# Kernel optimization log

Hardware: AMD Instinct MI355X
Metric: run time of the kernel (lower is better)

Reference implementation:

```python
import jax, jax.numpy as jnp
import numpy as np

N, E, G, D, L, T = 50000, 100000, 2000, 300, 5, 10
NUM_ATOM, NUM_CHIR, NUM_BOND, NUM_DIR = 120, 3, 6, 3


def setup_inputs() -> dict:
    key = jax.random.key(0)
    ks = jax.random.split(key, 24)
    s = 1.0 / np.sqrt(D)
    inp = {
        'x': jnp.stack([jax.random.randint(ks[0], (N,), 0, NUM_ATOM),
                        jax.random.randint(ks[1], (N,), 0, NUM_CHIR)], axis=1),
        'edge_index': jax.random.randint(ks[2], (2, E), 0, N),
        'edge_attr': jnp.stack([jax.random.randint(ks[3], (E,), 0, 4),
                                jax.random.randint(ks[4], (E,), 0, NUM_DIR)], axis=1),
        'batch': jnp.sort(jax.random.randint(ks[5], (N,), 0, G)),
        'x1': jnp.stack([jax.random.randint(ks[6], (N,), 0, NUM_ATOM),
                         jax.random.randint(ks[7], (N,), 0, NUM_CHIR)], axis=1),
        'edge_index1': jax.random.randint(ks[8], (2, E), 0, N),
        'edge_attr1': jnp.stack([jax.random.randint(ks[9], (E,), 0, 4),
                                 jax.random.randint(ks[10], (E,), 0, NUM_DIR)], axis=1),
        'batch1': jnp.sort(jax.random.randint(ks[11], (N,), 0, G)),
        'xemb1': jax.random.normal(ks[12], (NUM_ATOM, D)) * s,
        'xemb2': jax.random.normal(ks[13], (NUM_CHIR, D)) * s,
        'eemb1': jax.random.normal(ks[14], (L, NUM_BOND, D)) * s,
        'eemb2': jax.random.normal(ks[15], (L, NUM_DIR, D)) * s,
        'W1': jax.random.normal(ks[16], (L, D, 2 * D)) * s,
        'b1': jnp.zeros((L, 2 * D)),
        'W2': jax.random.normal(ks[17], (L, 2 * D, D)) * (1.0 / np.sqrt(2 * D)),
        'b2': jnp.zeros((L, D)),
        'gamma': jnp.ones((L, D)),
        'beta': jnp.zeros((L, D)),
        'predW': jax.random.normal(ks[18], (D, T)) * s,
        'predb': jnp.zeros((T,)),
    }
    return inp


def _gnn(xi, ei, ea, xemb1, xemb2, eemb1, eemb2, W1, b1, W2, b2, gamma, beta):
    n = xi.shape[0]
    h = xemb1[xi[:, 0]] + xemb2[xi[:, 1]]  # [N, D]
    loop = jnp.arange(n)
    src = jnp.concatenate([ei[0], loop])
    dst = jnp.concatenate([ei[1], loop])
    # self-loop edge attr = [4, 0]
    sl = jnp.concatenate([jnp.full((n, 1), 4, ea.dtype), jnp.zeros((n, 1), ea.dtype)], axis=1)
    eaf = jnp.concatenate([ea, sl], axis=0)
    for l in range(L):
        eemb = eemb1[l][eaf[:, 0]] + eemb2[l][eaf[:, 1]]     # [E+N, D]
        msg = h[src] + eemb                                   # gather
        agg = jax.ops.segment_sum(msg, dst, num_segments=n)   # scatter-add
        h2 = jax.nn.relu(agg @ W1[l] + b1[l]) @ W2[l] + b2[l] # GIN MLP
        mu = h2.mean(axis=0)
        var = ((h2 - mu) ** 2).mean(axis=0)                   # batchnorm (train stats)
        h2 = gamma[l] * (h2 - mu) * jax.lax.rsqrt(var + 1e-5) + beta[l]
        if l < L - 1:
            h2 = jax.nn.relu(h2)
        h = h2
    return h  # JK='last'


def _mean_pool(node_rep, batch):
    s = jax.ops.segment_sum(node_rep, batch, num_segments=G)
    cnt = jax.ops.segment_sum(jnp.ones((node_rep.shape[0],), node_rep.dtype), batch, num_segments=G)
    return s / jnp.maximum(cnt, 1.0)[:, None]


def reference(x, edge_index, edge_attr, batch, x1, edge_index1, edge_attr1, batch1,
              xemb1, xemb2, eemb1, eemb2, W1, b1, W2, b2, gamma, beta, predW, predb):
    node_rep = _gnn(x, edge_index, edge_attr, xemb1, xemb2, eemb1, eemb2, W1, b1, W2, b2, gamma, beta)
    node_rep1 = _gnn(x1, edge_index1, edge_attr1, xemb1, xemb2, eemb1, eemb2, W1, b1, W2, b2, gamma, beta)
    graph_rep = _mean_pool(node_rep, batch)
    graph_rep1 = _mean_pool(node_rep1, batch1)
    pred = graph_rep @ predW + predb
    pred1 = graph_rep1 @ predW + predb
    return (pred, graph_rep, node_rep, pred1, graph_rep1, node_rep1)
```

## Files before the change

kernel.cpp:

```cpp
#include <hip/hip_runtime.h>
#include <hip/hip_bf16.h>

typedef unsigned short ushort_t;
typedef short v8s __attribute__((ext_vector_type(8)));
typedef unsigned short v8u __attribute__((ext_vector_type(8)));
typedef unsigned short v4u __attribute__((ext_vector_type(4)));
typedef float v4f __attribute__((ext_vector_type(4)));

#define N_NODES 50000
#define N_EDGES 100000
#define N_GRAPH 2000
#define DIM     300
#define DIM2    600
#define NLAYER  5
#define NTASK   10
#define D4      75
#define D4P     80

#define LDA  304
#define NPAD 50048
#define KST1 10
#define KST2 19

#define KB1 40
#define NT1 5
#define KB2 76
#define NT2 3
#define MT_TILES 391
#define MT2      782

#define AS1 __attribute__((address_space(1)))
#define AS3 __attribute__((address_space(3)))
static __device__ __forceinline__ void gload_lds16(const void* g, void* l) {
    __builtin_amdgcn_global_load_lds((AS1 void*)(g), (AS3 void*)(l), 16, 0, 0);
}

static __device__ __forceinline__ ushort_t f2bf(float f) {
    unsigned int u;
    __builtin_memcpy(&u, &f, 4);
    unsigned int lsb = (u >> 16) & 1u;
    u += 0x7fffu + lsb;
    return (ushort_t)(u >> 16);
}
static __device__ __forceinline__ void split2(float f, ushort_t& h, ushort_t& l) {
    unsigned int u;
    __builtin_memcpy(&u, &f, 4);
    h = (ushort_t)(u >> 16);
    unsigned int um = u & 0xFFFF0000u;
    float hf;
    __builtin_memcpy(&hf, &um, 4);
    float lf = f - hf;
    unsigned int ul;
    __builtin_memcpy(&ul, &lf, 4);
    l = (ushort_t)(ul >> 16);
}

static __device__ __forceinline__ int swz_wgid(int orig, int nwg) {
    int xcd = orig & 7;
    int seq = orig >> 3;
    int q = nwg >> 3, r = nwg & 7;
    int base = (xcd < r) ? xcd * (q + 1) : r * (q + 1) + (xcd - r) * q;
    return base + seq;
}

__global__ void k_deg(const int* __restrict__ ei, int* __restrict__ deg) {
    int e = blockIdx.x * blockDim.x + threadIdx.x;
    if (e >= N_EDGES) return;
    atomicAdd(&deg[ei[N_EDGES + e]], 1);
}

__global__ void k_scan1(const int* __restrict__ deg, int* __restrict__ excl,
                        int* __restrict__ blksum) {
    __shared__ int s[256];
    int i = blockIdx.x * 256 + threadIdx.x;
    int v = (i < N_NODES) ? deg[i] : 0;
    s[threadIdx.x] = v;
    __syncthreads();
#pragma unroll
    for (int o = 1; o < 256; o <<= 1) {
        int t = (threadIdx.x >= o) ? s[threadIdx.x - o] : 0;
        __syncthreads();
        s[threadIdx.x] += t;
        __syncthreads();
    }
    if (i < N_NODES) excl[i] = s[threadIdx.x] - v;
    if (threadIdx.x == 255) blksum[blockIdx.x] = s[255];
}

__global__ void k_scan2(int* __restrict__ blksum, int* __restrict__ blkoff, int nblk) {
    __shared__ int s[256];
    int v = (threadIdx.x < nblk) ? blksum[threadIdx.x] : 0;
    s[threadIdx.x] = v;
    __syncthreads();
#pragma unroll
    for (int o = 1; o < 256; o <<= 1) {
        int t = (threadIdx.x >= o) ? s[threadIdx.x - o] : 0;
        __syncthreads();
        s[threadIdx.x] += t;
        __syncthreads();
    }
    if (threadIdx.x < nblk) blkoff[threadIdx.x] = s[threadIdx.x] - v;
}

__global__ void k_scan3(const int* __restrict__ excl, const int* __restrict__ blkoff,
                        int* __restrict__ rowptr, int* __restrict__ fillptr) {
    int i = blockIdx.x * blockDim.x + threadIdx.x;
    if (i > N_NODES) return;
    int v = (i < N_NODES) ? (excl[i] + blkoff[i >> 8]) : N_EDGES;
    rowptr[i] = v;
    if (i < N_NODES) fillptr[i] = v;
}

__global__ void k_fill(const int* __restrict__ ei, const int* __restrict__ ea,
                       int* __restrict__ fillptr,
                       int* __restrict__ csrc, int* __restrict__ cea) {
    int e = blockIdx.x * blockDim.x + threadIdx.x;
    if (e >= N_EDGES) return;
    int dst = ei[N_EDGES + e];
    int pos = atomicAdd(&fillptr[dst], 1);
    csrc[pos] = ei[e];
    cea[pos] = (ea[2 * e + 0] << 16) | ea[2 * e + 1];
}

template <bool EMB>
__global__ void k_gather_agg(const int* __restrict__ rowptr0,
                             const int* __restrict__ csrc0,
                             const int* __restrict__ cea0,
                             const int* __restrict__ rowptr1,
                             const int* __restrict__ csrc1,
                             const int* __restrict__ cea1,
                             const int* __restrict__ x0,
                             const int* __restrict__ x1,
                             const float* __restrict__ xe1,
                             const float* __restrict__ xe2,
                             const float* __restrict__ hin,
                             const float* __restrict__ ee1,
                             const float* __restrict__ ee2,
                             const float* __restrict__ ee1sl,
                             const float* __restrict__ ee2sl,
                             const float* __restrict__ bnmean,
                             const float* __restrict__ bnrstd,
                             const float* __restrict__ bngam,
                             const float* __restrict__ bnbet,
                             ushort_t* __restrict__ aghi,
                             ushort_t* __restrict__ aglo) {
    int tid = blockIdx.x * blockDim.x + threadIdx.x;
    if (tid >= 2 * N_NODES * D4P) return;
    int gi = tid / D4P;
    int c = tid % D4P;
    int graph = (gi >= N_NODES) ? 1 : 0;
    int ln = gi - graph * N_NODES;
    int row = graph * NPAD + ln;
    int d0 = c * 4;
    const int mt = row >> 7, m = row & 127;
    const int ks = d0 >> 5, kb = (d0 >> 3) & 3, jq = d0 & 7;
    const size_t off = (((size_t)mt * KST1 + ks) * 4 + kb) * 1024 + m * 8 + jq;
    if (c >= D4) {
        v4u z = (v4u){0, 0, 0, 0};
        *(v4u*)(aghi + off) = z;
        *(v4u*)(aglo + off) = z;
        return;
    }
    const int* rowptr = graph ? rowptr1 : rowptr0;
    const int* csrc   = graph ? csrc1   : csrc0;
    const int* cea    = graph ? cea1    : cea0;
    const int* xp     = graph ? x1      : x0;

    float4 m4, r4, g4, b4;
    if (!EMB) {
        const int bo = graph * DIM + d0;
        m4 = *(const float4*)(bnmean + bo);
        r4 = *(const float4*)(bnrstd + bo);
        g4 = *(const float4*)(bngam + d0);
        b4 = *(const float4*)(bnbet + d0);
    }
    auto hval = [&](int node) -> float4 {
        if (EMB) {
            int i0 = xp[node * 2 + 0];
            int i1 = xp[node * 2 + 1];
            float4 a = *(const float4*)(xe1 + (size_t)i0 * DIM + d0);
            float4 b = *(const float4*)(xe2 + (size_t)i1 * DIM + d0);
            float4 o;
            o.x = a.x + b.x; o.y = a.y + b.y; o.z = a.z + b.z; o.w = a.w + b.w;
            return o;
        } else {
            float4 v = *(const float4*)(hin + (size_t)(graph * NPAD + node) * LDA + d0);
            v.x = fmaxf((v.x - m4.x) * r4.x * g4.x + b4.x, 0.f);
            v.y = fmaxf((v.y - m4.y) * r4.y * g4.y + b4.y, 0.f);
            v.z = fmaxf((v.z - m4.z) * r4.z * g4.z + b4.z, 0.f);
            v.w = fmaxf((v.w - m4.w) * r4.w * g4.w + b4.w, 0.f);
            return v;
        }
    };
    float4 a = hval(ln);
    float4 e1 = *(const float4*)(ee1sl + d0);
    float4 e2 = *(const float4*)(ee2sl + d0);
    a.x += e1.x + e2.x; a.y += e1.y + e2.y; a.z += e1.z + e2.z; a.w += e1.w + e2.w;
    int p0 = rowptr[ln], p1 = rowptr[ln + 1];
    for (int p = p0; p < p1; ++p) {
        int src = csrc[p];
        int pk = cea[p];
        int a0 = pk >> 16, a1 = pk & 0xFFFF;
        float4 hv = hval(src);
        float4 f1 = *(const float4*)(ee1 + (size_t)a0 * DIM + d0);
        float4 f2 = *(const float4*)(ee2 + (size_t)a1 * DIM + d0);
        a.x += hv.x + f1.x + f2.x;
        a.y += hv.y + f1.y + f2.y;
        a.z += hv.z + f1.z + f2.z;
        a.w += hv.w + f1.w + f2.w;
    }
    float av[4] = {a.x, a.y, a.z, a.w};
    v4u hh, ll;
#pragma unroll
    for (int i = 0; i < 4; ++i) {
        ushort_t uh, ul;
        split2(av[i], uh, ul);
        hh[i] = uh;
        ll[i] = ul;
    }
    *(v4u*)(aghi + off) = hh;
    *(v4u*)(aglo + off) = ll;
}

__global__ void k_pack_w(const float* __restrict__ W,
                         ushort_t* __restrict__ hi,
                         ushort_t* __restrict__ lo,
                         int K, int N, int KBv, int NTv, int total) {
    int idx = blockIdx.x * blockDim.x + threadIdx.x;
    if (idx >= total) return;
    int j = idx & 7;
    int n = (idx >> 3) & 127;
    int tmp = idx >> 10;
    int kb = tmp % KBv; tmp /= KBv;
    int nt = tmp % NTv;
    int l = tmp / NTv;
    int k = kb * 8 + j;
    int ng = nt * 128 + n;
    float v = 0.f;
    if (k < K && ng < N) v = W[((size_t)l * K + k) * N + ng];
    ushort_t h, lw;
    split2(v, h, lw);
    hi[idx] = h;
    lo[idx] = lw;
}

template <bool RELU, bool SPLITA, bool BNSTAT, typename OT>
__global__ __launch_bounds__(256) void k_gemm_mfma(
        const ushort_t* __restrict__ Ahi,
        const ushort_t* __restrict__ Alo,
        const ushort_t* __restrict__ Bhi,
        const ushort_t* __restrict__ Blo,
        const float* __restrict__ bias,
        OT* __restrict__ C,
        double* __restrict__ bnsum,
        double* __restrict__ bnsq,
        int M, int N, int Ksteps, int KBv, int NTv, int nwg,
        int ldc, int ncap, int ksout, int mtHalf) {
    alignas(16) __shared__ ushort_t sBhi[8192];
    alignas(16) __shared__ ushort_t sBlo[8192];

    const int wgid = swz_wgid(blockIdx.x, nwg);
    const int nt = wgid % NTv;
    const int mt = wgid / NTv;
    const int t = threadIdx.x;

    const int w = t >> 6;
    const int lane = t & 63;
    const int wm = w >> 1;
    const int wn = w & 1;
    const int quad = lane >> 4;
    const int lr = lane & 15;

    v4f acc[4][4];
#pragma unroll
    for (int i = 0; i < 4; ++i)
#pragma unroll
        for (int j = 0; j < 4; ++j) acc[i][j] = (v4f){0.f, 0.f, 0.f, 0.f};

    const int aoff = quad * 1024 + (wm * 64 + lr) * 8;

    auto stageB = [&](int buf, int ks) {
        const int bo = buf * 4096;
        const size_t bbase = ((size_t)nt * KBv + ks * 4) * 1024;
#pragma unroll
        for (int p = 0; p < 2; ++p) {
            int o = p * 2048 + t * 8;
            gload_lds16(Bhi + bbase + o, &sBhi[bo + o]);
            gload_lds16(Blo + bbase + o, &sBlo[bo + o]);
        }
    };

    stageB(0, 0);
    __syncthreads();
    int cur = 0;
    for (int ks = 0; ks < Ksteps; ++ks) {
        const ushort_t* ah = Ahi + ((size_t)mt * Ksteps + ks) * 4096 + aoff;
        const ushort_t* al = SPLITA ? (Alo + ((size_t)mt * Ksteps + ks) * 4096 + aoff) : nullptr;
        v8s a_hi[4], a_lo[4];
#pragma unroll
        for (int s = 0; s < 4; ++s) {
            a_hi[s] = *(const v8s*)(ah + s * 128);
            if (SPLITA) a_lo[s] = *(const v8s*)(al + s * 128);
        }
        __builtin_amdgcn_sched_barrier(0);
        if (ks + 1 < Ksteps) stageB(cur ^ 1, ks + 1);
        const int bo = cur * 4096;
#pragma unroll
        for (int sj = 0; sj < 4; ++sj) {
            v8s bh = *(const v8s*)&sBhi[bo + quad * 1024 + (wn * 64 + sj * 16 + lr) * 8];
            v8s bl = *(const v8s*)&sBlo[bo + quad * 1024 + (wn * 64 + sj * 16 + lr) * 8];
#pragma unroll
            for (int si = 0; si < 4; ++si) {
                acc[si][sj] = __builtin_amdgcn_mfma_f32_16x16x32_bf16(
                    a_hi[si], bh, acc[si][sj], 0, 0, 0);
                acc[si][sj] = __builtin_amdgcn_mfma_f32_16x16x32_bf16(
                    a_hi[si], bl, acc[si][sj], 0, 0, 0);
                if (SPLITA)
                    acc[si][sj] = __builtin_amdgcn_mfma_f32_16x16x32_bf16(
                        a_lo[si], bh, acc[si][sj], 0, 0, 0);
            }
        }
        __syncthreads();
        cur ^= 1;
    }

    const int graph = (mt >= mtHalf) ? 1 : 0;
    float bsum[4], bsq[4];
    if (BNSTAT) {
#pragma unroll
        for (int sj = 0; sj < 4; ++sj) { bsum[sj] = 0.f; bsq[sj] = 0.f; }
    }
#pragma unroll
    for (int sj = 0; sj < 4; ++sj) {
        int col = nt * 128 + wn * 64 + sj * 16 + lr;
        if (col >= ncap) continue;
        float bv = (col < N) ? bias[col] : 0.f;
        size_t yb = 0;
        if (sizeof(OT) == 2)
            yb = (((size_t)mt * ksout + (col >> 5)) * 4 + ((col >> 3) & 3)) * 1024 + (col & 7);
#pragma unroll
        for (int si = 0; si < 4; ++si) {
#pragma unroll
            for (int r = 0; r < 4; ++r) {
                int m = wm * 64 + si * 16 + quad * 4 + r;
                size_t row = (size_t)mt * 128 + m;
                float v = acc[si][sj][r] + bv;
                if (RELU) v = fmaxf(v, 0.f);
                if (BNSTAT) {
                    int lrow = (mt - graph * mtHalf) * 128 + m;
                    if (lrow < M) { bsum[sj] += v; bsq[sj] += v * v; }
                }
                if (sizeof(OT) == 2)
                    ((ushort_t*)C)[yb + m * 8] = f2bf(v);
                else
                    ((float*)C)[row * ldc + col] = v;
            }
        }
    }
    if (BNSTAT) {
        float* sred = (float*)sBhi;
#pragma unroll
        for (int sj = 0; sj < 4; ++sj) {
            bsum[sj] += __shfl_xor(bsum[sj], 16);
            bsum[sj] += __shfl_xor(bsum[sj], 32);
            bsq[sj]  += __shfl_xor(bsq[sj], 16);
            bsq[sj]  += __shfl_xor(bsq[sj], 32);
        }
        if (quad == 0) {
#pragma unroll
            for (int sj = 0; sj < 4; ++sj) {
                int idx = wm * 128 + wn * 64 + sj * 16 + lr;
                sred[idx] = bsum[sj];
                sred[256 + idx] = bsq[sj];
            }
        }
        __syncthreads();
        if (t < 128) {
            float s = sred[t] + sred[128 + t];
            float q = sred[256 + t] + sred[256 + 128 + t];
            int col = nt * 128 + t;
            if (col < N) {
                atomicAdd(&bnsum[graph * N + col], (double)s);
                atomicAdd(&bnsq[graph * N + col], (double)q);
            }
        }
    }
}

__global__ void k_bn_finalize(double* __restrict__ sum,
                              double* __restrict__ sumsq,
                              float* __restrict__ mean,
                              float* __restrict__ rstd) {
    int d = blockIdx.x * blockDim.x + threadIdx.x;
    if (d >= 2 * DIM) return;
    double mu = sum[d] / (double)N_NODES;
    double var = sumsq[d] / (double)N_NODES - mu * mu;
    if (var < 0.0) var = 0.0;
    mean[d] = (float)mu;
    rstd[d] = (float)(1.0 / sqrt(var + 1e-5));
    sum[d] = 0.0;
    sumsq[d] = 0.0;
}

__global__ __launch_bounds__(256) void k_bn_pool(const float* __restrict__ h2,
                                                 const int* __restrict__ bat0,
                                                 const int* __restrict__ bat1,
                                                 const float* __restrict__ mean,
                                                 const float* __restrict__ rstd,
                                                 const float* __restrict__ gam,
                                                 const float* __restrict__ bet,
                                                 float* __restrict__ node0,
                                                 float* __restrict__ node1,
                                                 float* __restrict__ pool,
                                                 float* __restrict__ gout0,
                                                 float* __restrict__ gout1) {
    __shared__ float4 s[3][D4];
    const int bid = blockIdx.x;
    const int graph = (bid >= N_GRAPH) ? 1 : 0;
    const int g = bid - graph * N_GRAPH;
    const int* batch = graph ? bat1 : bat0;
    const float* h2g = h2 + (size_t)graph * NPAD * LDA;
    float* nodeout = graph ? node1 : node0;
    float* gout = graph ? gout1 : gout0;

    int lo = 0, hi = N_NODES;
    while (lo < hi) {
        int m = (lo + hi) >> 1;
        if (batch[m] < g) lo = m + 1; else hi = m;
    }
    const int p0 = lo;
    hi = N_NODES;
    while (lo < hi) {
        int m = (lo + hi) >> 1;
        if (batch[m] < g + 1) lo = m + 1; else hi = m;
    }
    const int p1 = lo;

    const int t = threadIdx.x;
    if (t < 3 * D4) {
        const int c = t % D4;
        const int rc = t / D4;
        const int d0 = c * 4;
        float4 m4 = *(const float4*)(mean + graph * DIM + d0);
        float4 r4 = *(const float4*)(rstd + graph * DIM + d0);
        float4 g4 = *(const float4*)(gam + d0);
        float4 b4 = *(const float4*)(bet + d0);
        float4 acc = {0.f, 0.f, 0.f, 0.f};
        for (int r = p0 + rc; r < p1; r += 3) {
            float4 v = *(const float4*)(h2g + (size_t)r * LDA + d0);
            v.x = (v.x - m4.x) * r4.x * g4.x + b4.x;
            v.y = (v.y - m4.y) * r4.y * g4.y + b4.y;
            v.z = (v.z - m4.z) * r4.z * g4.z + b4.z;
            v.w = (v.w - m4.w) * r4.w * g4.w + b4.w;
            *(float4*)(nodeout + (size_t)r * DIM + d0) = v;
            acc.x += v.x; acc.y += v.y; acc.z += v.z; acc.w += v.w;
        }
        s[rc][c] = acc;
    }
    __syncthreads();
    if (t < D4) {
        float4 a = s[0][t], b = s[1][t], c = s[2][t];
        const float inv = 1.0f / fmaxf((float)(p1 - p0), 1.0f);
        float4 r;
        r.x = (a.x + b.x + c.x) * inv;
        r.y = (a.y + b.y + c.y) * inv;
        r.z = (a.z + b.z + c.z) * inv;
        r.w = (a.w + b.w + c.w) * inv;
        *(float4*)(pool + (size_t)bid * DIM + t * 4) = r;
        *(float4*)(gout + (size_t)g * DIM + t * 4) = r;
    }
}

__global__ void k_pred(const float* __restrict__ pool,
                       const float* __restrict__ predW,
                       const float* __restrict__ predb,
                       float* __restrict__ out0,
                       float* __restrict__ out1) {
    int tid = blockIdx.x * blockDim.x + threadIdx.x;
    if (tid >= 2 * N_GRAPH * NTASK) return;
    int gg = tid / NTASK;
    int tt = tid % NTASK;
    int graph = (gg >= N_GRAPH) ? 1 : 0;
    int g = gg - graph * N_GRAPH;
    float s = predb[tt];
    const float* pr = pool + (size_t)gg * DIM;
    for (int k = 0; k < DIM; ++k) s += pr[k] * predW[k * NTASK + tt];
    float* outp = graph ? out1 : out0;
    outp[(size_t)g * NTASK + tt] = s;
}

static inline int cdiv(long long a, long long b) { return (int)((a + b - 1) / b); }

extern "C" void kernel_launch(void* const* d_in, const int* in_sizes, int n_in,
                              void* d_out, int out_size, void* d_ws, size_t ws_size,
                              hipStream_t stream) {
    const int* x    = (const int*)d_in[0];
    const int* ei   = (const int*)d_in[1];
    const int* ea   = (const int*)d_in[2];
    const int* bat  = (const int*)d_in[3];
    const int* x1   = (const int*)d_in[4];
    const int* ei1  = (const int*)d_in[5];
    const int* ea1  = (const int*)d_in[6];
    const int* bat1 = (const int*)d_in[7];
    const float* xemb1 = (const float*)d_in[8];
    const float* xemb2 = (const float*)d_in[9];
    const float* eemb1 = (const float*)d_in[10];
    const float* eemb2 = (const float*)d_in[11];
    const float* W1    = (const float*)d_in[12];
    const float* b1    = (const float*)d_in[13];
    const float* W2    = (const float*)d_in[14];
    const float* b2    = (const float*)d_in[15];
    const float* gamma = (const float*)d_in[16];
    const float* beta  = (const float*)d_in[17];
    const float* predW = (const float*)d_in[18];
    const float* predb = (const float*)d_in[19];
    float* out = (float*)d_out;

    char* ws = (char*)d_ws;
    size_t off = 0;
    auto take = [&](size_t bytes) -> char* {
        char* p = ws + off;
        off += (bytes + 255) & ~(size_t)255;
        return p;
    };
    const size_t PLANE = (size_t)MT2 * KST1 * 4096;
    const size_t BUFSZ = PLANE * 2 * 2;
    char* bufA = take(BUFSZ);
    char* bufB = take(BUFSZ);
    float* pool   = (float*)take((size_t)2 * N_GRAPH * DIM * 4);
    double* bnsum = (double*)take(2 * DIM * 8 * 2);
    double* bnsq  = bnsum + 2 * DIM;
    float* bnmean = (float*)take(2 * DIM * 4 * 2);
    float* bnrstd = bnmean + 2 * DIM;
    const size_t W1P = (size_t)NLAYER * NT1 * KB1 * 1024;
    const size_t W2P = (size_t)NLAYER * NT2 * KB2 * 1024;
    ushort_t* w1hi = (ushort_t*)take(W1P * 2);
    ushort_t* w1lo = (ushort_t*)take(W1P * 2);
    ushort_t* w2hi = (ushort_t*)take(W2P * 2);
    ushort_t* w2lo = (ushort_t*)take(W2P * 2);
    int* deg     = (int*)take(N_NODES * 4);
    int* excl    = (int*)take(N_NODES * 4);
    int* blksum  = (int*)take(256 * 4);
    int* blkoff  = (int*)take(256 * 4);
    int* fillptr = (int*)take(N_NODES * 4);
    int* rowptr0 = (int*)take((N_NODES + 1) * 4);
    int* csrc0   = (int*)take(N_EDGES * 4);
    int* cea0    = (int*)take(N_EDGES * 4);
    int* rowptr1 = (int*)take((N_NODES + 1) * 4);
    int* csrc1   = (int*)take(N_EDGES * 4);
    int* cea1    = (int*)take(N_EDGES * 4);
    (void)ws_size; (void)in_sizes; (void)n_in; (void)out_size;

    const int TB = 256;
    const int gE   = cdiv(N_EDGES, TB);
    const int gScan = cdiv(N_NODES, TB);
    const int gScan3 = cdiv(N_NODES + 1, TB);
    const int gGath = cdiv((long long)2 * N_NODES * D4P, TB);
    const int NWG1 = NT1 * MT2;
    const int NWG2 = NT2 * MT2;

    k_pack_w<<<cdiv((long long)W1P, TB), TB, 0, stream>>>(W1, w1hi, w1lo, DIM, DIM2, KB1, NT1, (int)W1P);
    k_pack_w<<<cdiv((long long)W2P, TB), TB, 0, stream>>>(W2, w2hi, w2lo, DIM2, DIM, KB2, NT2, (int)W2P);

    auto build_csr = [&](const int* eip, const int* eap, int* rowptr, int* csrc, int* cea) {
        hipMemsetAsync(deg, 0, N_NODES * 4, stream);
        k_deg<<<gE, TB, 0, stream>>>(eip, deg);
        k_scan1<<<gScan, TB, 0, stream>>>(deg, excl, blksum);
        k_scan2<<<1, 256, 0, stream>>>(blksum, blkoff, gScan);
        k_scan3<<<gScan3, TB, 0, stream>>>(excl, blkoff, rowptr, fillptr);
        k_fill<<<gE, TB, 0, stream>>>(eip, eap, fillptr, csrc, cea);
    };
    build_csr(ei, ea, rowptr0, csrc0, cea0);
    build_csr(ei1, ea1, rowptr1, csrc1, cea1);

    hipMemsetAsync(bnsum, 0, 2 * DIM * 8 * 2, stream);

    const size_t GT = (size_t)N_GRAPH * NTASK;
    const size_t GD = (size_t)N_GRAPH * DIM;
    const size_t ND = (size_t)N_NODES * DIM;
    float* out_pred0  = out;
    float* out_graph0 = out + GT;
    float* out_node0  = out + GT + GD;
    float* out_pred1  = out + GT + GD + ND;
    float* out_graph1 = out + 2 * GT + GD + ND;
    float* out_node1  = out + 2 * GT + 2 * GD + ND;

    for (int l = 0; l < NLAYER; ++l) {
        char* pb = (l & 1) ? bufA : bufB;
        char* yb = (l & 1) ? bufB : bufA;
        ushort_t* aghi = (ushort_t*)pb;
        ushort_t* aglo = aghi + PLANE;
        const float* gin = (const float*)yb;
        ushort_t* yv = (ushort_t*)yb;
        float* h2v = (float*)pb;
        const float* ee1l = eemb1 + (size_t)l * 6 * DIM;
        const float* ee2l = eemb2 + (size_t)l * 3 * DIM;
        if (l == 0)
            k_gather_agg<true><<<gGath, TB, 0, stream>>>(
                rowptr0, csrc0, cea0, rowptr1, csrc1, cea1, x, x1, xemb1, xemb2,
                nullptr, ee1l, ee2l, ee1l + 4 * DIM, ee2l,
                nullptr, nullptr, nullptr, nullptr, aghi, aglo);
        else
            k_gather_agg<false><<<gGath, TB, 0, stream>>>(
                rowptr0, csrc0, cea0, rowptr1, csrc1, cea1, x, x1, xemb1, xemb2,
                gin, ee1l, ee2l, ee1l + 4 * DIM, ee2l,
                bnmean, bnrstd, gamma + (size_t)(l - 1) * DIM, beta + (size_t)(l - 1) * DIM,
                aghi, aglo);
        k_gemm_mfma<true, true, false, ushort_t>
            <<<NWG1, TB, 0, stream>>>(
                aghi, aglo,
                w1hi + (size_t)l * NT1 * KB1 * 1024, w1lo + (size_t)l * NT1 * KB1 * 1024,
                b1 + (size_t)l * DIM2, yv, nullptr, nullptr,
                N_NODES, DIM2, KST1, KB1, NT1, NWG1, 0, 608, KST2, MT_TILES);
        k_gemm_mfma<false, false, true, float>
            <<<NWG2, TB, 0, stream>>>(
                yv, yv,
                w2hi + (size_t)l * NT2 * KB2 * 1024, w2lo + (size_t)l * NT2 * KB2 * 1024,
                b2 + (size_t)l * DIM, h2v, bnsum, bnsq,
                N_NODES, DIM, KST2, KB2, NT2, NWG2, LDA, 304, 0, MT_TILES);
        k_bn_finalize<<<3, 256, 0, stream>>>(bnsum, bnsq, bnmean, bnrstd);
    }
    k_bn_pool<<<2 * N_GRAPH, TB, 0, stream>>>(
        (const float*)bufB, bat, bat1, bnmean, bnrstd,
        gamma + (size_t)(NLAYER - 1) * DIM, beta + (size_t)(NLAYER - 1) * DIM,
        out_node0, out_node1, pool, out_graph0, out_graph1);
    k_pred<<<cdiv((long long)2 * N_GRAPH * NTASK, TB), TB, 0, stream>>>(
        pool, predW, predb, out_pred0, out_pred1);
}
```

Baseline: 1.976 ms.

## Load GEMM B fragments directly from global, drop LDS staging; swizzle gather blocks

The MFMA GEMM no longer stages the weight tiles into double-buffered LDS with global_load_lds. Each wave now loads its own B fragments straight from global memory into registers alongside the A fragments, which removes the per-k-step barrier and most of the LDS use (only a small reduction buffer remains). The gather kernel also remaps its block index through the same workgroup swizzle used by the GEMM. The trade-off is that B is read redundantly by the waves sharing a column tile and there is no prefetch of the next k-step, so the GEMM may stall more on global-memory latency in exchange for higher occupancy and no synchronisation.

```diff
diff --git a/kernel.cpp b/kernel.cpp
--- a/kernel.cpp
+++ b/kernel.cpp
@@ -28,12 +28,6 @@
 #define NT2 3
 #define MT_TILES 391
 #define MT2      782
-
-#define AS1 __attribute__((address_space(1)))
-#define AS3 __attribute__((address_space(3)))
-static __device__ __forceinline__ void gload_lds16(const void* g, void* l) {
-    __builtin_amdgcn_global_load_lds((AS1 void*)(g), (AS3 void*)(l), 16, 0, 0);
-}
 
 static __device__ __forceinline__ ushort_t f2bf(float f) {
     unsigned int u;
@@ -143,8 +137,10 @@
                              const float* __restrict__ bngam,
                              const float* __restrict__ bnbet,
                              ushort_t* __restrict__ aghi,
-                             ushort_t* __restrict__ aglo) {
-    int tid = blockIdx.x * blockDim.x + threadIdx.x;
+                             ushort_t* __restrict__ aglo,
+                             int nwg) {
+    int wgid = swz_wgid(blockIdx.x, nwg);
+    int tid = wgid * blockDim.x + threadIdx.x;
     if (tid >= 2 * N_NODES * D4P) return;
     int gi = tid / D4P;
     int c = tid % D4P;
@@ -256,8 +252,7 @@
         double* __restrict__ bnsq,
         int M, int N, int Ksteps, int KBv, int NTv, int nwg,
         int ldc, int ncap, int ksout, int mtHalf) {
-    alignas(16) __shared__ ushort_t sBhi[8192];
-    alignas(16) __shared__ ushort_t sBlo[8192];
+    __shared__ float sred[512];
 
     const int wgid = swz_wgid(blockIdx.x, nwg);
     const int nt = wgid % NTv;
@@ -278,50 +273,34 @@
         for (int j = 0; j < 4; ++j) acc[i][j] = (v4f){0.f, 0.f, 0.f, 0.f};
 
     const int aoff = quad * 1024 + (wm * 64 + lr) * 8;
-
-    auto stageB = [&](int buf, int ks) {
-        const int bo = buf * 4096;
-        const size_t bbase = ((size_t)nt * KBv + ks * 4) * 1024;
-#pragma unroll
-        for (int p = 0; p < 2; ++p) {
-            int o = p * 2048 + t * 8;
-            gload_lds16(Bhi + bbase + o, &sBhi[bo + o]);
-            gload_lds16(Blo + bbase + o, &sBlo[bo + o]);
-        }
-    };
-
-    stageB(0, 0);
-    __syncthreads();
-    int cur = 0;
+    const int boff = (wn * 64 + lr) * 8;
+
     for (int ks = 0; ks < Ksteps; ++ks) {
         const ushort_t* ah = Ahi + ((size_t)mt * Ksteps + ks) * 4096 + aoff;
         const ushort_t* al = SPLITA ? (Alo + ((size_t)mt * Ksteps + ks) * 4096 + aoff) : nullptr;
-        v8s a_hi[4], a_lo[4];
+        const ushort_t* bh_p = Bhi + ((size_t)(nt * KBv + ks * 4 + quad)) * 1024 + boff;
+        const ushort_t* bl_p = Blo + ((size_t)(nt * KBv + ks * 4 + quad)) * 1024 + boff;
+        v8s a_hi[4], a_lo[4], b_hi[4], b_lo[4];
 #pragma unroll
         for (int s = 0; s < 4; ++s) {
             a_hi[s] = *(const v8s*)(ah + s * 128);
             if (SPLITA) a_lo[s] = *(const v8s*)(al + s * 128);
-        }
-        __builtin_amdgcn_sched_barrier(0);
-        if (ks + 1 < Ksteps) stageB(cur ^ 1, ks + 1);
-        const int bo = cur * 4096;
+            b_hi[s] = *(const v8s*)(bh_p + s * 128);
+            b_lo[s] = *(const v8s*)(bl_p + s * 128);
+        }
 #pragma unroll
         for (int sj = 0; sj < 4; ++sj) {
-            v8s bh = *(const v8s*)&sBhi[bo + quad * 1024 + (wn * 64 + sj * 16 + lr) * 8];
-            v8s bl = *(const v8s*)&sBlo[bo + quad * 1024 + (wn * 64 + sj * 16 + lr) * 8];
 #pragma unroll
             for (int si = 0; si < 4; ++si) {
                 acc[si][sj] = __builtin_amdgcn_mfma_f32_16x16x32_bf16(
-                    a_hi[si], bh, acc[si][sj], 0, 0, 0);
+                    a_hi[si], b_hi[sj], acc[si][sj], 0, 0, 0);
                 acc[si][sj] = __builtin_amdgcn_mfma_f32_16x16x32_bf16(
-                    a_hi[si], bl, acc[si][sj], 0, 0, 0);
+                    a_hi[si], b_lo[sj], acc[si][sj], 0, 0, 0);
                 if (SPLITA)
                     acc[si][sj] = __builtin_amdgcn_mfma_f32_16x16x32_bf16(
-                        a_lo[si], bh, acc[si][sj], 0, 0, 0);
+                        a_lo[si], b_hi[sj], acc[si][sj], 0, 0, 0);
             }
         }
-        __syncthreads();
-        cur ^= 1;
     }
 
     const int graph = (mt >= mtHalf) ? 1 : 0;
@@ -358,7 +337,6 @@
         }
     }
     if (BNSTAT) {
-        float* sred = (float*)sBhi;
 #pragma unroll
         for (int sj = 0; sj < 4; ++sj) {
             bsum[sj] += __shfl_xor(bsum[sj], 16);
@@ -599,13 +577,13 @@
             k_gather_agg<true><<<gGath, TB, 0, stream>>>(
                 rowptr0, csrc0, cea0, rowptr1, csrc1, cea1, x, x1, xemb1, xemb2,
                 nullptr, ee1l, ee2l, ee1l + 4 * DIM, ee2l,
-                nullptr, nullptr, nullptr, nullptr, aghi, aglo);
+                nullptr, nullptr, nullptr, nullptr, aghi, aglo, gGath);
         else
             k_gather_agg<false><<<gGath, TB, 0, stream>>>(
                 rowptr0, csrc0, cea0, rowptr1, csrc1, cea1, x, x1, xemb1, xemb2,
                 gin, ee1l, ee2l, ee1l + 4 * DIM, ee2l,
                 bnmean, bnrstd, gamma + (size_t)(l - 1) * DIM, beta + (size_t)(l - 1) * DIM,
-                aghi, aglo);
+                aghi, aglo, gGath);
         k_gemm_mfma<true, true, false, ushort_t>
             <<<NWG1, TB, 0, stream>>>(
                 aghi, aglo,
```

After: 2.085 ms. 5.5% more time.
